# Kernel tuning notes

Hardware: AMD Instinct MI355X
Metric: run time of the kernel (lower is better)

The kernel has to match this reference:

```python
import jax, jax.numpy as jnp
import numpy as np

BIG_NUMBER = 1000000.0
B, N, H = 4, 512, 128   # batch, nodes, feature dim
MID, OUT = 128, 128
Z_DIM = 2 * H           # concat(node_fts, hidden)


def _glorot(key, fan_in, fan_out):
    s = 1.0 / np.sqrt(fan_in)
    return jax.random.truncated_normal(key, -2.0, 2.0, (fan_in, fan_out), jnp.float32) * s


def setup_inputs() -> dict:
    key = jax.random.key(0)
    ks = jax.random.split(key, 12)
    inp = {
        "node_fts": jax.random.normal(ks[0], (B, N, H), jnp.float32),
        "edge_fts": jax.random.normal(ks[1], (B, N, N, H), jnp.float32),
        "graph_fts": jax.random.normal(ks[2], (B, H), jnp.float32),
        "adj_mat": jax.random.randint(ks[3], (B, N, N), 0, 2, jnp.int32),
        "hidden": jax.random.normal(ks[4], (B, N, H), jnp.float32),
        # Linear params (hk.Linear: y = x @ W + b)
        "W_m1": _glorot(ks[5], Z_DIM, MID), "b_m1": jnp.zeros((MID,), jnp.float32),
        "W_m2": _glorot(ks[6], Z_DIM, MID), "b_m2": jnp.zeros((MID,), jnp.float32),
        "W_me": _glorot(ks[7], H, MID),     "b_me": jnp.zeros((MID,), jnp.float32),
        "W_mg": _glorot(ks[8], H, MID),     "b_mg": jnp.zeros((MID,), jnp.float32),
        "W_o1": _glorot(ks[9], Z_DIM, OUT), "b_o1": jnp.zeros((OUT,), jnp.float32),
        "W_o2": _glorot(ks[10], MID, OUT),  "b_o2": jnp.zeros((OUT,), jnp.float32),
    }
    return inp


def reference(node_fts, edge_fts, graph_fts, adj_mat, hidden,
              W_m1, b_m1, W_m2, b_m2, W_me, b_me, W_mg, b_mg,
              W_o1, b_o1, W_o2, b_o2):
    # z: [b, n, 2h]
    z = jnp.concatenate([node_fts, hidden], axis=-1)
    msg_1 = z @ W_m1 + b_m1                       # [b, n, mid] (source j)
    msg_2 = z @ W_m2 + b_m2                       # [b, n, mid] (target i)
    msg_e = edge_fts @ W_me + b_me                # [b, n, n, mid]
    msg_g = graph_fts @ W_mg + b_mg               # [b, mid]
    # msgs[b, j, i, :] = msg_1[b, i] + msg_2[b, j] + msg_e[b, j, i] + msg_g[b]
    msgs = (msg_1[:, None, :, :] + msg_2[:, :, None, :]
            + msg_e + msg_g[:, None, None, :])    # [b, n, n, mid]
    # masked max over axis=1 (aggregation over senders)
    mask = (adj_mat != 0)[..., None]               # [b, n, n, 1]
    maxarg = jnp.where(mask, msgs, -BIG_NUMBER)
    agg = jnp.max(maxarg, axis=1)                  # [b, n, mid]
    ret = (z @ W_o1 + b_o1) + (agg @ W_o2 + b_o2)  # [b, n, out]
    return jax.nn.relu(ret)
```

## Files before the change

kernel.cpp:

```cpp
#include <hip/hip_runtime.h>
#include <hip/hip_bf16.h>


#define BN 4
#define NN 512
#define HH 128
#define MIDD 128
#define ZD 256
#define JCN 8
#define JPB 64
#define TI 32

typedef __attribute__((ext_vector_type(8))) short bf16x8;
typedef __attribute__((ext_vector_type(4))) float f32x4;

static __device__ __forceinline__ unsigned short f2bf(float f) {
  union { __hip_bfloat16 h; unsigned short u; } cv;
  cv.h = __float2bfloat16(f);
  return cv.u;
}
static __device__ __forceinline__ unsigned pack2(float a, float b) {
  return (unsigned)f2bf(a) | ((unsigned)f2bf(b) << 16);
}

__global__ __launch_bounds__(256) void phaseA(
    const float* __restrict__ node, const float* __restrict__ hidden,
    const float* __restrict__ graph,
    const float* __restrict__ Wm1, const float* __restrict__ bm1,
    const float* __restrict__ Wm2, const float* __restrict__ bm2,
    const float* __restrict__ bme,
    const float* __restrict__ Wmg, const float* __restrict__ bmg,
    const float* __restrict__ Wo1, const float* __restrict__ bo1,
    float* __restrict__ s2, float* __restrict__ cst, float* __restrict__ front)
{
  __shared__ float zsh[8][ZD];
  __shared__ float mg[MIDD];
  const int t = threadIdx.x;
  const int r0 = blockIdx.x * 8;
  const int b = r0 / NN;

  #pragma unroll
  for (int s = 0; s < 8; ++s) {
    const int row = r0 + s;
    zsh[s][t] = (t < HH) ? node[(size_t)row * HH + t]
                         : hidden[(size_t)row * HH + (t - HH)];
  }
  if (t < MIDD) {
    float a = bmg[t];
    #pragma unroll 4
    for (int k = 0; k < HH; ++k) a += graph[b * HH + k] * Wmg[k * MIDD + t];
    mg[t] = a;
  }
  __syncthreads();

  const int c = t & 127;
  const int rh = t >> 7;
  float a2[4] = {0, 0, 0, 0}, a1[4] = {0, 0, 0, 0}, ao[4] = {0, 0, 0, 0};
  #pragma unroll 4
  for (int k = 0; k < ZD; ++k) {
    const float w2 = Wm2[k * MIDD + c];
    const float w1 = Wm1[k * MIDD + c];
    const float wo = Wo1[k * MIDD + c];
    #pragma unroll
    for (int q = 0; q < 4; ++q) {
      const float zv = zsh[rh * 4 + q][k];
      a2[q] += zv * w2; a1[q] += zv * w1; ao[q] += zv * wo;
    }
  }
  #pragma unroll
  for (int q = 0; q < 4; ++q) {
    const size_t row = r0 + rh * 4 + q;
    s2[row * MIDD + c]    = a2[q] + bm2[c] + bme[c];
    cst[row * MIDD + c]   = a1[q] + bm1[c] + mg[c];
    front[row * MIDD + c] = ao[q] + bo1[c];
  }
}

__global__ __launch_bounds__(256, 2) void mainK(
    const float* __restrict__ edge, const int* __restrict__ adj,
    const float* __restrict__ Wme, const float* __restrict__ s2,
    float* __restrict__ partial)
{
  __shared__ __align__(16) unsigned short ash[2][TI][HH + 8];
  __shared__ unsigned bits[JPB];

  const int tid = threadIdx.x;
  const int wv = tid >> 6, lane = tid & 63;
  const int quad = lane >> 4, l15 = lane & 15;
  const int bx = blockIdx.x;
  const int it = bx & 15, jc = (bx >> 4) & 7, b = bx >> 7;
  const int i0 = it * TI, jb = jc * JPB;

  bf16x8 bf[2][4];
  #pragma unroll
  for (int sm = 0; sm < 2; ++sm) {
    #pragma unroll
    for (int ks = 0; ks < 4; ++ks) {
      union { bf16x8 v; unsigned short u[8]; } tmp;
      const int m = wv * 32 + sm * 16 + l15;
      #pragma unroll
      for (int e = 0; e < 8; ++e) {
        const int k = ks * 32 + quad * 8 + e;
        tmp.u[e] = f2bf(Wme[k * MIDD + m]);
      }
      bf[sm][ks] = tmp.v;
    }
  }

  for (int q = 0; q < 8; ++q) {
    const int jl = wv * 16 + q * 2 + (lane >> 5);
    const int i = i0 + (lane & 31);
    const int pred = adj[((size_t)(b * NN + jb + jl)) * NN + i] != 0;
    const unsigned long long m = __ballot(pred);
    if (lane == 0)  bits[jl] = (unsigned)m;
    if (lane == 32) bits[jl] = (unsigned)(m >> 32);
  }

  f32x4 acc[2][2];
  #pragma unroll
  for (int si = 0; si < 2; ++si)
    #pragma unroll
    for (int sm = 0; sm < 2; ++sm)
      acc[si][sm] = f32x4{-1e6f, -1e6f, -1e6f, -1e6f};

  float4 pf[4];
  {
    const float* p = edge + (((size_t)(b * NN + jb)) * NN + i0) * HH;
    #pragma unroll
    for (int s = 0; s < 4; ++s) pf[s] = *(const float4*)(p + s * 1024 + tid * 4);
    #pragma unroll
    for (int s = 0; s < 4; ++s) {
      const int e = s * 1024 + tid * 4;
      *(uint2*)&ash[0][e >> 7][e & 127] =
          make_uint2(pack2(pf[s].x, pf[s].y), pack2(pf[s].z, pf[s].w));
    }
  }

  const float* s2row = s2 + ((size_t)(b * NN + jb)) * MIDD;

  for (int jj = 0; jj < JPB; ++jj) {
    const int cur = jj & 1;
    __syncthreads();

    if (jj + 1 < JPB) {
      const float* p = edge + (((size_t)(b * NN + jb + jj + 1)) * NN + i0) * HH;
      #pragma unroll
      for (int s = 0; s < 4; ++s) pf[s] = *(const float4*)(p + s * 1024 + tid * 4);
    }

    const unsigned mb = bits[jj];
    const float s2v0 = s2row[jj * MIDD + wv * 32 + l15];
    const float s2v1 = s2row[jj * MIDD + wv * 32 + 16 + l15];

    #pragma unroll
    for (int si = 0; si < 2; ++si) {
      bf16x8 af[4];
      #pragma unroll
      for (int ks = 0; ks < 4; ++ks)
        af[ks] = *(const bf16x8*)&ash[cur][si * 16 + l15][ks * 32 + quad * 8];
      #pragma unroll
      for (int sm = 0; sm < 2; ++sm) {
        f32x4 d = {0.f, 0.f, 0.f, 0.f};
        #pragma unroll
        for (int ks = 0; ks < 4; ++ks)
          d = __builtin_amdgcn_mfma_f32_16x16x32_bf16(af[ks], bf[sm][ks], d, 0, 0, 0);
        const float sv = sm ? s2v1 : s2v0;
        #pragma unroll
        for (int r = 0; r < 4; ++r) {
          const int ip = si * 16 + quad * 4 + r;
          const float v = d[r] + sv;
          if ((mb >> ip) & 1u) acc[si][sm][r] = fmaxf(acc[si][sm][r], v);
        }
      }
    }

    if (jj + 1 < JPB) {
      #pragma unroll
      for (int s = 0; s < 4; ++s) {
        const int e = s * 1024 + tid * 4;
        *(uint2*)&ash[cur ^ 1][e >> 7][e & 127] =
            make_uint2(pack2(pf[s].x, pf[s].y), pack2(pf[s].z, pf[s].w));
      }
    }
  }

  float* pb = partial + ((size_t)jc * (BN * NN) + b * NN + i0) * MIDD;
  #pragma unroll
  for (int si = 0; si < 2; ++si)
    #pragma unroll
    for (int sm = 0; sm < 2; ++sm)
      #pragma unroll
      for (int r = 0; r < 4; ++r) {
        const int ip = si * 16 + quad * 4 + r;
        const int m = wv * 32 + sm * 16 + l15;
        pb[(size_t)ip * MIDD + m] = acc[si][sm][r];
      }
}

__global__ __launch_bounds__(256) void combineK(
    const float* __restrict__ partial, const float* __restrict__ cst,
    const float* __restrict__ front, const float* __restrict__ Wo2,
    const float* __restrict__ bo2, float* __restrict__ out)
{
  __shared__ float agg[8][MIDD];
  const int t = threadIdx.x;
  const int c = t & 127, h = t >> 7;
  const int r0 = blockIdx.x * 8;

  for (int rr = h; rr < 8; rr += 2) {
    const size_t row = r0 + rr;
    float v = -1e6f;
    #pragma unroll
    for (int p = 0; p < JCN; ++p)
      v = fmaxf(v, partial[((size_t)p * (BN * NN) + row) * MIDD + c]);
    agg[rr][c] = (v > -9.0e5f) ? (v + cst[row * MIDD + c]) : -1e6f;
  }
  __syncthreads();

  float a[4];
  #pragma unroll
  for (int q = 0; q < 4; ++q) {
    const size_t row = r0 + h * 4 + q;
    a[q] = front[row * MIDD + c] + bo2[c];
  }
  #pragma unroll 4
  for (int k = 0; k < MIDD; ++k) {
    const float w = Wo2[k * MIDD + c];
    #pragma unroll
    for (int q = 0; q < 4; ++q) a[q] += agg[h * 4 + q][k] * w;
  }
  #pragma unroll
  for (int q = 0; q < 4; ++q) {
    const size_t row = r0 + h * 4 + q;
    out[row * MIDD + c] = fmaxf(a[q], 0.f);
  }
}

extern "C" void kernel_launch(void* const* d_in, const int* in_sizes, int n_in,
                              void* d_out, int out_size, void* d_ws, size_t ws_size,
                              hipStream_t stream)
{
  const float* node   = (const float*)d_in[0];
  const float* edge   = (const float*)d_in[1];
  const float* graph  = (const float*)d_in[2];
  const int*   adj    = (const int*)d_in[3];
  const float* hidden = (const float*)d_in[4];
  const float* Wm1 = (const float*)d_in[5];
  const float* bm1 = (const float*)d_in[6];
  const float* Wm2 = (const float*)d_in[7];
  const float* bm2 = (const float*)d_in[8];
  const float* Wme = (const float*)d_in[9];
  const float* bme = (const float*)d_in[10];
  const float* Wmg = (const float*)d_in[11];
  const float* bmg = (const float*)d_in[12];
  const float* Wo1 = (const float*)d_in[13];
  const float* bo1 = (const float*)d_in[14];
  const float* Wo2 = (const float*)d_in[15];
  const float* bo2 = (const float*)d_in[16];

  float* ws      = (float*)d_ws;
  float* s2      = ws;
  float* cst     = ws + 262144;
  float* front   = ws + 524288;
  float* partial = ws + 786432;
  float* out     = (float*)d_out;

  phaseA<<<256, 256, 0, stream>>>(node, hidden, graph, Wm1, bm1, Wm2, bm2, bme,
                                  Wmg, bmg, Wo1, bo1, s2, cst, front);
  mainK<<<512, 256, 0, stream>>>(edge, adj, Wme, s2, partial);
  combineK<<<256, 256, 0, stream>>>(partial, cst, front, Wo2, bo2, out);
}
```

Before: 792.0 us.

## Load edge fragments straight into registers, drop LDS staging and per-step barriers

The main kernel no longer stages each edge row through a double-buffered LDS tile. Instead every wave loads its own MFMA A-fragments directly from global memory, converts them to bf16 in registers, and the per-iteration __syncthreads is gone. The s2 rows for the block's j-range are preloaded into LDS once. The aim is to remove LDS write/read traffic and barrier stalls. The cost is that each of the 4 waves reloads the same edge data (4x global/L2 reads), and there is no explicit prefetch of the next row.

Result: slower. 915.4 us (+15.6%).

```diff
diff --git a/kernel.cpp b/kernel.cpp
--- a/kernel.cpp
+++ b/kernel.cpp
@@ -81,7 +81,7 @@
     const float* __restrict__ Wme, const float* __restrict__ s2,
     float* __restrict__ partial)
 {
-  __shared__ __align__(16) unsigned short ash[2][TI][HH + 8];
+  __shared__ float s2sh[JPB * MIDD];
   __shared__ unsigned bits[JPB];
 
   const int tid = threadIdx.x;
@@ -104,6 +104,15 @@
         tmp.u[e] = f2bf(Wme[k * MIDD + m]);
       }
       bf[sm][ks] = tmp.v;
+    }
+  }
+
+  {
+    const float* s2g = s2 + ((size_t)(b * NN + jb)) * MIDD;
+    #pragma unroll
+    for (int s = 0; s < 8; ++s) {
+      const int idx = s * 1024 + tid * 4;
+      *(float4*)&s2sh[idx] = *(const float4*)(s2g + idx);
     }
   }
 
@@ -116,6 +125,8 @@
     if (lane == 32) bits[jl] = (unsigned)(m >> 32);
   }
 
+  __syncthreads();
+
   f32x4 acc[2][2];
   #pragma unroll
   for (int si = 0; si < 2; ++si)
@@ -123,41 +134,38 @@
     for (int sm = 0; sm < 2; ++sm)
       acc[si][sm] = f32x4{-1e6f, -1e6f, -1e6f, -1e6f};
 
-  float4 pf[4];
-  {
-    const float* p = edge + (((size_t)(b * NN + jb)) * NN + i0) * HH;
-    #pragma unroll
-    for (int s = 0; s < 4; ++s) pf[s] = *(const float4*)(p + s * 1024 + tid * 4);
-    #pragma unroll
-    for (int s = 0; s < 4; ++s) {
-      const int e = s * 1024 + tid * 4;
-      *(uint2*)&ash[0][e >> 7][e & 127] =
-          make_uint2(pack2(pf[s].x, pf[s].y), pack2(pf[s].z, pf[s].w));
-    }
-  }
-
-  const float* s2row = s2 + ((size_t)(b * NN + jb)) * MIDD;
+  const float* ebase = edge + (((size_t)(b * NN + jb)) * NN + i0) * HH;
 
   for (int jj = 0; jj < JPB; ++jj) {
-    const int cur = jj & 1;
-    __syncthreads();
-
-    if (jj + 1 < JPB) {
-      const float* p = edge + (((size_t)(b * NN + jb + jj + 1)) * NN + i0) * HH;
-      #pragma unroll
-      for (int s = 0; s < 4; ++s) pf[s] = *(const float4*)(p + s * 1024 + tid * 4);
+    const float* rowp = ebase + (size_t)jj * NN * HH;
+
+    float4 pa[2][4][2];
+    #pragma unroll
+    for (int si = 0; si < 2; ++si) {
+      const float* rp = rowp + (size_t)(si * 16 + l15) * HH + quad * 8;
+      #pragma unroll
+      for (int ks = 0; ks < 4; ++ks) {
+        pa[si][ks][0] = *(const float4*)(rp + ks * 32);
+        pa[si][ks][1] = *(const float4*)(rp + ks * 32 + 4);
+      }
     }
 
     const unsigned mb = bits[jj];
-    const float s2v0 = s2row[jj * MIDD + wv * 32 + l15];
-    const float s2v1 = s2row[jj * MIDD + wv * 32 + 16 + l15];
+    const float s2v0 = s2sh[jj * MIDD + wv * 32 + l15];
+    const float s2v1 = s2sh[jj * MIDD + wv * 32 + 16 + l15];
 
     #pragma unroll
     for (int si = 0; si < 2; ++si) {
       bf16x8 af[4];
       #pragma unroll
-      for (int ks = 0; ks < 4; ++ks)
-        af[ks] = *(const bf16x8*)&ash[cur][si * 16 + l15][ks * 32 + quad * 8];
+      for (int ks = 0; ks < 4; ++ks) {
+        union { bf16x8 v; unsigned u4[4]; } t;
+        t.u4[0] = pack2(pa[si][ks][0].x, pa[si][ks][0].y);
+        t.u4[1] = pack2(pa[si][ks][0].z, pa[si][ks][0].w);
+        t.u4[2] = pack2(pa[si][ks][1].x, pa[si][ks][1].y);
+        t.u4[3] = pack2(pa[si][ks][1].z, pa[si][ks][1].w);
+        af[ks] = t.v;
+      }
       #pragma unroll
       for (int sm = 0; sm < 2; ++sm) {
         f32x4 d = {0.f, 0.f, 0.f, 0.f};
@@ -171,15 +179,6 @@
           const float v = d[r] + sv;
           if ((mb >> ip) & 1u) acc[si][sm][r] = fmaxf(acc[si][sm][r], v);
         }
-      }
-    }
-
-    if (jj + 1 < JPB) {
-      #pragma unroll
-      for (int s = 0; s < 4; ++s) {
-        const int e = s * 1024 + tid * 4;
-        *(uint2*)&ash[cur ^ 1][e >> 7][e & 127] =
-            make_uint2(pack2(pf[s].x, pf[s].y), pack2(pf[s].z, pf[s].w));
       }
     }
   }
```
